# Kernel tuning notes

Hardware: AMD Instinct MI355X
Metric: run time of the kernel (lower is better)

## Reference

```python
import jax, jax.numpy as jnp
import numpy as np

B, S, HID = 2, 1024, 4096
NQ, NG, D = 32, 4, 128
NKV = NQ // NG  # 8 kv heads
OFF = 1024


def setup_inputs() -> dict:
    key = jax.random.key(0)
    ks = jax.random.split(key, 13)
    w = 0.02
    return {
        "x": jax.random.normal(ks[0], (B, S, HID), jnp.float32),
        "offset": OFF,
        "precomp_freqs_cos": jax.random.uniform(ks[1], (S, D // 2), jnp.float32, -1.0, 1.0),
        "precomp_freqs_sin": jax.random.uniform(ks[2], (S, D // 2), jnp.float32, -1.0, 1.0),
        "k_cache": jax.random.normal(ks[3], (B, OFF, NQ, D), jnp.float32),
        "v_cache": jax.random.normal(ks[4], (B, OFF, NQ, D), jnp.float32),
        "q_w": jax.random.normal(ks[5], (NQ * D, HID), jnp.float32) * w,
        "q_b": jax.random.normal(ks[6], (NQ * D,), jnp.float32) * w,
        "k_w": jax.random.normal(ks[7], (NKV * D, HID), jnp.float32) * w,
        "k_b": jax.random.normal(ks[8], (NKV * D,), jnp.float32) * w,
        "v_w": jax.random.normal(ks[9], (NKV * D, HID), jnp.float32) * w,
        "v_b": jax.random.normal(ks[10], (NKV * D,), jnp.float32) * w,
        "o_w": jax.random.normal(ks[11], (HID, NQ * D), jnp.float32) * w,
    }


def _rope(x, cos, sin):
    # x: [b, s, h, d]; cos/sin: [s, d//2] applied to interleaved pairs
    b, s, h, d = x.shape
    xp = x.reshape(b, s, h, d // 2, 2)
    xr, xi = xp[..., 0], xp[..., 1]
    c = cos[None, :, None, :]
    sn = sin[None, :, None, :]
    out = jnp.stack([xr * c - xi * sn, xr * sn + xi * c], axis=-1)
    return out.reshape(b, s, h, d)


def reference(x, offset, precomp_freqs_cos, precomp_freqs_sin, k_cache, v_cache,
              q_w, q_b, k_w, k_b, v_w, v_b, o_w):
    b, s, _ = x.shape
    q = (x @ q_w.T + q_b).reshape(b, s, NQ, D)
    k = (x @ k_w.T + k_b).reshape(b, s, NKV, D)
    v = (x @ v_w.T + v_b).reshape(b, s, NKV, D)
    # GQA expansion: '(hr)' -> each kv head repeated NG times contiguously
    k = jnp.repeat(k, NG, axis=2)  # [b, s, NQ, D]
    v = jnp.repeat(v, NG, axis=2)
    q = _rope(q, precomp_freqs_cos, precomp_freqs_sin)
    k = _rope(k, precomp_freqs_cos, precomp_freqs_sin)
    k = jnp.concatenate([k_cache, k], axis=1)  # [b, offset+s, NQ, D]
    v = jnp.concatenate([v_cache, v], axis=1)
    qk = jnp.einsum('bsnd,btnd->bnst', q, k) / np.float32(np.sqrt(D))
    neg_inf = jnp.asarray(-jnp.inf, qk.dtype)
    causal = jnp.triu(jnp.full((s, s), neg_inf, qk.dtype), k=1)
    mask = jnp.concatenate([jnp.zeros((s, offset), qk.dtype), causal], axis=1)
    qk = qk + mask[None, None, :, :]
    p = jax.nn.softmax(qk, axis=-1)
    out = jnp.einsum('bnst,btnd->bsnd', p, v).reshape(b, s, NQ * D)
    out = out @ o_w.T
    return (out, k, v)
```

## Files before the change

kernel.cpp:

```cpp
#include <hip/hip_runtime.h>
#include <hip/hip_bf16.h>
#include <cstdio>
#include <cstdint>

typedef __bf16 bf16_t;
typedef __bf16 bf16x8 __attribute__((ext_vector_type(8)));
typedef float f32x4 __attribute__((ext_vector_type(4)));

static constexpr int Bc = 2, Sc = 1024, HIDc = 4096;
static constexpr int NQc = 32, NKVc = 8, Dc = 128, OFFc = 1024, Tc = 2048;
static constexpr int Mrows = Bc * Sc;
static constexpr int NQKV = (NQc + 2 * NKVc) * Dc;

__device__ inline void load_lds16(const void* g, void* l) {
    __builtin_amdgcn_global_load_lds(
        (const __attribute__((address_space(1))) unsigned*)g,
        (__attribute__((address_space(3))) unsigned*)l, 16, 0, 0);
}

__global__ void k_cvt(const float* __restrict__ src, bf16_t* __restrict__ dst, long n4) {
    long i = blockIdx.x * (long)blockDim.x + threadIdx.x;
    long stride = (long)gridDim.x * blockDim.x;
    const float4* s4 = (const float4*)src;
    for (; i < n4; i += stride) {
        float4 v = s4[i];
        bf16_t t[4] = {(bf16_t)v.x, (bf16_t)v.y, (bf16_t)v.z, (bf16_t)v.w};
        *(uint2*)&dst[i * 4] = *(uint2*)t;
    }
}

template <bool BIAS, bool OUT_BF16>
__global__ __launch_bounds__(256) void k_gemm(const bf16_t* __restrict__ A,
                                              const bf16_t* __restrict__ Bm,
                                              const float* __restrict__ bias,
                                              void* __restrict__ Cout,
                                              int M, int N, int K) {
    __shared__ __align__(16) bf16_t As[128][32];
    __shared__ __align__(16) bf16_t Bs[128][32];
    const int tid = threadIdx.x, wid = tid >> 6, lane = tid & 63;
    const int g = lane >> 4, ln = lane & 15;
    const int wm = wid >> 1, wn = wid & 1;
    const int gx = gridDim.x;
    int bidl = blockIdx.y * gx + blockIdx.x;
    int cpx = (gx * gridDim.y) >> 3;
    int swz = (bidl & 7) * cpx + (bidl >> 3);
    const int m0 = (swz / gx) * 128, n0 = (swz % gx) * 128;
    f32x4 acc[4][4] = {};

    for (int k0 = 0; k0 < K; k0 += 32) {
        __syncthreads();
#pragma unroll
        for (int c = 0; c < 2; ++c) {
            int row = wid * 32 + c * 16 + (lane >> 2);
            int col = (lane & 3) * 8;
            load_lds16(A + (size_t)(m0 + row) * K + k0 + col, &As[wid * 32 + c * 16][0]);
            load_lds16(Bm + (size_t)(n0 + row) * K + k0 + col, &Bs[wid * 32 + c * 16][0]);
        }
        __syncthreads();
        bf16x8 af[4], bfr[4];
#pragma unroll
        for (int i = 0; i < 4; ++i) af[i] = *(const bf16x8*)&As[wm * 64 + i * 16 + ln][g * 8];
#pragma unroll
        for (int i = 0; i < 4; ++i) bfr[i] = *(const bf16x8*)&Bs[wn * 64 + i * 16 + ln][g * 8];
#pragma unroll
        for (int i = 0; i < 4; ++i)
#pragma unroll
            for (int j = 0; j < 4; ++j)
                acc[i][j] = __builtin_amdgcn_mfma_f32_16x16x32_bf16(af[i], bfr[j], acc[i][j], 0, 0, 0);
    }

#pragma unroll
    for (int i = 0; i < 4; ++i) {
#pragma unroll
        for (int j = 0; j < 4; ++j) {
            int col = n0 + wn * 64 + j * 16 + ln;
            float bv = BIAS ? bias[col] : 0.f;
#pragma unroll
            for (int r = 0; r < 4; ++r) {
                int row = m0 + wm * 64 + i * 16 + g * 4 + r;
                float v = acc[i][j][r] + bv;
                if (OUT_BF16)
                    ((bf16_t*)Cout)[(size_t)row * N + col] = (bf16_t)v;
                else
                    ((float*)Cout)[(size_t)row * N + col] = v;
            }
        }
    }
}

__global__ void k_rope_q(bf16_t* __restrict__ qkv, const float* __restrict__ cosT,
                         const float* __restrict__ sinT) {
    int row = blockIdx.x;
    int s = row & 1023;
    bf16_t* src = qkv + (size_t)row * NQKV;
    for (int p = threadIdx.x; p < 2048; p += 256) {
        int j = p & 63;
        float c = cosT[s * 64 + j], sn = sinT[s * 64 + j];
        float xr = (float)src[2 * p], xi = (float)src[2 * p + 1];
        src[2 * p]     = (bf16_t)(xr * c - xi * sn);
        src[2 * p + 1] = (bf16_t)(xr * sn + xi * c);
    }
}


__global__ __launch_bounds__(256) void k_ropekv(const bf16_t* __restrict__ qkv,
                                                const float* __restrict__ cosT,
                                                const float* __restrict__ sinT,
                                                float* __restrict__ out_k,
                                                float* __restrict__ out_v,
                                                bf16_t* __restrict__ kfr,
                                                bf16_t* __restrict__ vfr) {
    __shared__ __align__(16) bf16_t Vl[64][136];
    const int sb = blockIdx.x, hk = blockIdx.y, b = blockIdx.z;
    const int tid = threadIdx.x;
    const int tt = tid >> 2, dq = (tid & 3) * 32;
    const int s = sb * 64 + tt;
    const int t = OFFc + s;
    const bf16_t* krow = qkv + (size_t)(b * Sc + s) * NQKV + NQc * Dc + hk * Dc + dq;
    const bf16_t* vrow = qkv + (size_t)(b * Sc + s) * NQKV + (NQc + NKVc) * Dc + hk * Dc + dq;

    float cs[16], sn[16];
    int j0 = dq >> 1;
#pragma unroll
    for (int q4 = 0; q4 < 4; ++q4) {
        float4 cv = *(const float4*)&cosT[s * 64 + j0 + q4 * 4];
        float4 sv = *(const float4*)&sinT[s * 64 + j0 + q4 * 4];
        cs[q4 * 4] = cv.x; cs[q4 * 4 + 1] = cv.y; cs[q4 * 4 + 2] = cv.z; cs[q4 * 4 + 3] = cv.w;
        sn[q4 * 4] = sv.x; sn[q4 * 4 + 1] = sv.y; sn[q4 * 4 + 2] = sv.z; sn[q4 * 4 + 3] = sv.w;
    }

    bf16_t kb[32], vb[32];
#pragma unroll
    for (int c = 0; c < 4; ++c) {
        *(uint4*)&kb[c * 8] = *(const uint4*)&krow[c * 8];
        *(uint4*)&vb[c * 8] = *(const uint4*)&vrow[c * 8];
    }
    float ko[32], vo[32];
    bf16_t kbf[32];
#pragma unroll
    for (int jj = 0; jj < 16; ++jj) {
        float xr = (float)kb[2 * jj], xi = (float)kb[2 * jj + 1];
        ko[2 * jj]     = xr * cs[jj] - xi * sn[jj];
        ko[2 * jj + 1] = xr * sn[jj] + xi * cs[jj];
        kbf[2 * jj]     = (bf16_t)ko[2 * jj];
        kbf[2 * jj + 1] = (bf16_t)ko[2 * jj + 1];
        vo[2 * jj] = (float)vb[2 * jj];
        vo[2 * jj + 1] = (float)vb[2 * jj + 1];
    }

    const int t16 = t >> 4, lnr = t & 15, dc = dq >> 5;
#pragma unroll
    for (int gg = 0; gg < 4; ++gg) {
        int hq = hk * 4 + gg;
        size_t o = ((size_t)(b * Tc + t) * NQc + hq) * Dc + dq;
#pragma unroll
        for (int c = 0; c < 8; ++c) {
            *(float4*)&out_k[o + c * 4] = *(float4*)&ko[c * 4];
            *(float4*)&out_v[o + c * 4] = *(float4*)&vo[c * 4];
        }
        size_t fb = ((size_t)b * NQc + hq) * ((size_t)Tc * Dc);
#pragma unroll
        for (int g = 0; g < 4; ++g)
            *(uint4*)&kfr[fb + (size_t)(((t16 * 4 + dc) * 4 + g) * 128 + lnr * 8)] = *(uint4*)&kbf[g * 8];
    }
#pragma unroll
    for (int c = 0; c < 4; ++c) *(uint4*)&Vl[tt][dq + c * 8] = *(uint4*)&vb[c * 8];
    __syncthreads();
    const int tile = 16 + sb;
#pragma unroll
    for (int i = 0; i < 4; ++i) {
        int u = i * 256 + tid;
        int d = u >> 3, cc = u & 7;
        bf16_t tmp[8];
#pragma unroll
        for (int j = 0; j < 8; ++j) tmp[j] = Vl[cc * 8 + j][d];
        size_t off = (size_t)((((tile * 8 + (d >> 4)) * 2 + (cc >> 2)) * 4 + (cc & 3)) * 128 + (d & 15) * 8);
#pragma unroll
        for (int gg = 0; gg < 4; ++gg) {
            int hq = hk * 4 + gg;
            size_t fb = ((size_t)b * NQc + hq) * ((size_t)Tc * Dc);
            *(uint4*)&vfr[fb + off] = *(uint4*)tmp;
        }
    }
}

__global__ __launch_bounds__(256) void k_cache(const float* __restrict__ kc,
                                               const float* __restrict__ vc,
                                               float* __restrict__ out_k,
                                               float* __restrict__ out_v,
                                               bf16_t* __restrict__ kfr,
                                               bf16_t* __restrict__ vfr) {
    __shared__ __align__(16) bf16_t Vl[64][136];
    const int tb = blockIdx.x, h = blockIdx.y, b = blockIdx.z;
    const int tid = threadIdx.x;
    const int tt = tid >> 2, dq = (tid & 3) * 32;
    const int t = tb * 64 + tt;
    size_t src = ((size_t)(b * OFFc + t) * NQc + h) * Dc + dq;
    size_t dst = ((size_t)(b * Tc + t) * NQc + h) * Dc + dq;
    const size_t fb = ((size_t)b * NQc + h) * ((size_t)Tc * Dc);

    bf16_t kb[32], vb[32];
#pragma unroll
    for (int c = 0; c < 8; ++c) {
        float4 kv = *(const float4*)&kc[src + c * 4];
        *(float4*)&out_k[dst + c * 4] = kv;
        kb[c * 4] = (bf16_t)kv.x; kb[c * 4 + 1] = (bf16_t)kv.y;
        kb[c * 4 + 2] = (bf16_t)kv.z; kb[c * 4 + 3] = (bf16_t)kv.w;
        float4 vv = *(const float4*)&vc[src + c * 4];
        *(float4*)&out_v[dst + c * 4] = vv;
        vb[c * 4] = (bf16_t)vv.x; vb[c * 4 + 1] = (bf16_t)vv.y;
        vb[c * 4 + 2] = (bf16_t)vv.z; vb[c * 4 + 3] = (bf16_t)vv.w;
    }
    const int t16 = t >> 4, lnr = t & 15, dc = dq >> 5;
#pragma unroll
    for (int g = 0; g < 4; ++g)
        *(uint4*)&kfr[fb + (size_t)(((t16 * 4 + dc) * 4 + g) * 128 + lnr * 8)] = *(uint4*)&kb[g * 8];

#pragma unroll
    for (int c = 0; c < 4; ++c) *(uint4*)&Vl[tt][dq + c * 8] = *(uint4*)&vb[c * 8];
    __syncthreads();
#pragma unroll
    for (int i = 0; i < 4; ++i) {
        int u = i * 256 + tid;
        int d = u >> 3, cc = u & 7;
        bf16_t tmp[8];
#pragma unroll
        for (int j = 0; j < 8; ++j) tmp[j] = Vl[cc * 8 + j][d];
        size_t off = (size_t)((((tb * 8 + (d >> 4)) * 2 + (cc >> 2)) * 4 + (cc & 3)) * 128 + (d & 15) * 8);
        *(uint4*)&vfr[fb + off] = *(uint4*)tmp;
    }
}

__global__ __launch_bounds__(512) void k_attn(const bf16_t* __restrict__ qkv,
                                              const bf16_t* __restrict__ kfr,
                                              const bf16_t* __restrict__ vfr,
                                              bf16_t* __restrict__ attn) {
    __shared__ __align__(16) bf16_t Kl[2][8192];
    __shared__ __align__(16) bf16_t Vl2[2][8192];
    __shared__ __align__(16) bf16_t Pl[8][32 * 72];
    const int tid = threadIdx.x, w = tid >> 6, l = tid & 63;
    const int g = l >> 4, ln = l & 15;
    const int bid = blockIdx.x;
    const int xcd = bid & 7, within = bid >> 3;
    const int qblk = 3 - (within & 3);
    const int u = within >> 2;
    const int b = u >> 2;
    const int h = (u & 3) * 8 + xcd;
    const int q0b = qblk * 256;
    const int qw0 = q0b + w * 32;
    const float SCALE = 0.08838834764831845f;
    const float L2E = 1.4426950408889634f;
    const size_t hb = ((size_t)b * NQc + h) * ((size_t)Tc * Dc);
    const bf16_t* kb = kfr + hb;
    const bf16_t* vb = vfr + hb;
    bf16_t* Pw = &Pl[w][0];

    bf16x8 qf[2][4];
#pragma unroll
    for (int mf = 0; mf < 2; ++mf) {
        size_t qrow = (size_t)(b * Sc + qw0 + mf * 16 + ln) * NQKV + h * Dc;
#pragma unroll
        for (int dc = 0; dc < 4; ++dc) qf[mf][dc] = *(const bf16x8*)&qkv[qrow + dc * 32 + g * 8];
    }
    f32x4 o[2][8] = {};
    float mrun[2] = {-1e30f, -1e30f};
    float lrun[2] = {0.f, 0.f};

    const int ntiles = (OFFc + q0b + 256) >> 6;

    auto stage = [&](int bf, int t) {
        const bf16_t* ksrc = kb + (size_t)t * 8192 + (size_t)(w * 2) * 512;
        const bf16_t* vsrc = vb + (size_t)t * 8192 + (size_t)(w * 2) * 512;
        load_lds16(ksrc + (size_t)l * 8,       &Kl[bf][(w * 2) * 512]);
        load_lds16(ksrc + 512 + (size_t)l * 8, &Kl[bf][(w * 2 + 1) * 512]);
        load_lds16(vsrc + (size_t)l * 8,       &Vl2[bf][(w * 2) * 512]);
        load_lds16(vsrc + 512 + (size_t)l * 8, &Vl2[bf][(w * 2 + 1) * 512]);
    };

    stage(0, 0);
    __syncthreads();
    int cur = 0;

    for (int t = 0; t < ntiles; ++t) {
        if (t + 1 < ntiles) stage(cur ^ 1, t + 1);
        f32x4 sa[2][4] = {};
#pragma unroll
        for (int nf = 0; nf < 4; ++nf) {
            bf16x8 kf[4];
#pragma unroll
            for (int dc = 0; dc < 4; ++dc)
                kf[dc] = *(const bf16x8*)&Kl[cur][((nf * 4 + dc) * 4 + g) * 128 + ln * 8];
#pragma unroll
            for (int dc = 0; dc < 4; ++dc) {
                sa[0][nf] = __builtin_amdgcn_mfma_f32_16x16x32_bf16(kf[dc], qf[0][dc], sa[0][nf], 0, 0, 0);
                sa[1][nf] = __builtin_amdgcn_mfma_f32_16x16x32_bf16(kf[dc], qf[1][dc], sa[1][nf], 0, 0, 0);
            }
        }
        bool maybe = (t * 64 + 63 > OFFc + qw0);
#pragma unroll
        for (int mf = 0; mf < 2; ++mf)
#pragma unroll
            for (int nf = 0; nf < 4; ++nf)
#pragma unroll
                for (int r = 0; r < 4; ++r) {
                    float s = sa[mf][nf][r] * SCALE;
                    if (maybe) {
                        int tg = t * 64 + nf * 16 + g * 4 + r;
                        int qg = qw0 + mf * 16 + ln;
                        if (tg > OFFc + qg) s = -1e30f;
                    }
                    sa[mf][nf][r] = s;
                }
        float tm[2];
        int grew = 0;
#pragma unroll
        for (int mf = 0; mf < 2; ++mf) {
            float m2 = sa[mf][0][0];
#pragma unroll
            for (int nf = 0; nf < 4; ++nf)
#pragma unroll
                for (int r = 0; r < 4; ++r) m2 = fmaxf(m2, sa[mf][nf][r]);
            m2 = fmaxf(m2, __shfl_xor(m2, 16));
            m2 = fmaxf(m2, __shfl_xor(m2, 32));
            tm[mf] = m2;
            grew |= (m2 > mrun[mf]) ? 1 : 0;
        }
        if (__any(grew)) {
#pragma unroll
            for (int mf = 0; mf < 2; ++mf) {
                float mn = fmaxf(mrun[mf], tm[mf]);
                float al = exp2f((mrun[mf] - mn) * L2E);
                mrun[mf] = mn;
                lrun[mf] *= al;
                float alr[4];
#pragma unroll
                for (int r = 0; r < 4; ++r)
                    alr[r] = __shfl(al, (l & 48) | (g * 4 + r));
#pragma unroll
                for (int df = 0; df < 8; ++df) {
                    f32x4 t4 = o[mf][df];
                    t4[0] *= alr[0]; t4[1] *= alr[1]; t4[2] *= alr[2]; t4[3] *= alr[3];
                    o[mf][df] = t4;
                }
            }
        }
#pragma unroll
        for (int mf = 0; mf < 2; ++mf) {
            const int qrow = mf * 16 + ln;
            float ps = 0.f;
#pragma unroll
            for (int nf = 0; nf < 4; ++nf) {
                bf16_t pv[4];
#pragma unroll
                for (int r = 0; r < 4; ++r) {
                    float p = exp2f((sa[mf][nf][r] - mrun[mf]) * L2E);
                    ps += p;
                    pv[r] = (bf16_t)p;
                }
                *(uint2*)&Pw[qrow * 72 + nf * 16 + g * 4] = *(uint2*)pv;
            }
            ps += __shfl_xor(ps, 16);
            ps += __shfl_xor(ps, 32);
            lrun[mf] += ps;
        }
#pragma unroll
        for (int kc = 0; kc < 2; ++kc) {
            bf16x8 vf[8];
#pragma unroll
            for (int df = 0; df < 8; ++df)
                vf[df] = *(const bf16x8*)&Vl2[cur][((df * 2 + kc) * 4 + g) * 128 + ln * 8];
#pragma unroll
            for (int mf = 0; mf < 2; ++mf) {
                bf16x8 pa = *(const bf16x8*)&Pw[(mf * 16 + ln) * 72 + kc * 32 + g * 8];
#pragma unroll
                for (int df = 0; df < 8; ++df)
                    o[mf][df] = __builtin_amdgcn_mfma_f32_16x16x32_bf16(pa, vf[df], o[mf][df], 0, 0, 0);
            }
        }
        __syncthreads();
        cur ^= 1;
    }

#pragma unroll
    for (int mf = 0; mf < 2; ++mf) {
        float linv[4];
#pragma unroll
        for (int r = 0; r < 4; ++r)
            linv[r] = 1.f / __shfl(lrun[mf], (l & 48) | (g * 4 + r));
#pragma unroll
        for (int df = 0; df < 8; ++df)
#pragma unroll
            for (int r = 0; r < 4; ++r) {
                float v = o[mf][df][r] * linv[r];
                size_t orow = (size_t)(b * Sc + qw0 + mf * 16 + g * 4 + r) * (NQc * Dc) + h * Dc + df * 16 + ln;
                attn[orow] = (bf16_t)v;
            }
    }
}

extern "C" void kernel_launch(void* const* d_in, const int* in_sizes, int n_in,
                              void* d_out, int out_size, void* d_ws, size_t ws_size,
                              hipStream_t stream) {
    const float* x      = (const float*)d_in[0];
    const float* cosT   = (const float*)d_in[2];
    const float* sinT   = (const float*)d_in[3];
    const float* kcache = (const float*)d_in[4];
    const float* vcache = (const float*)d_in[5];
    const float* q_w    = (const float*)d_in[6];
    const float* q_b    = (const float*)d_in[7];
    const float* k_w    = (const float*)d_in[8];
    const float* k_b    = (const float*)d_in[9];
    const float* v_w    = (const float*)d_in[10];
    const float* v_b    = (const float*)d_in[11];
    const float* o_w    = (const float*)d_in[12];

    char* ws = (char*)d_ws;
    size_t off = 0;
    auto alloc = [&](size_t bytes) {
        void* p = ws + off;
        off += (bytes + 255) & ~(size_t)255;
        return p;
    };
    bf16_t* xb   = (bf16_t*)alloc((size_t)Mrows * HIDc * 2);
    bf16_t* wqkv = (bf16_t*)alloc((size_t)Bc * Tc * NQc * Dc * 4);
    bf16_t* owb  = (bf16_t*)alloc((size_t)HIDc * HIDc * 2);
    bf16_t* qkv  = (bf16_t*)alloc((size_t)Mrows * NQKV * 2);
    float*  bias = (float*)alloc((size_t)NQKV * 4);
    if (off > ws_size) {
        fprintf(stderr, "WS too small: need %zu have %zu\n", off, ws_size);
        return;
    }
    bf16_t* attn  = xb;
    bf16_t* kfr = wqkv;
    bf16_t* vfr = wqkv + (size_t)Bc * NQc * Tc * Dc;

    float* out_o = (float*)d_out;
    float* out_k = out_o + (size_t)Mrows * HIDc;
    float* out_v = out_k + (size_t)Bc * Tc * NQc * Dc;

    k_cvt<<<2048, 256, 0, stream>>>(x, xb, (long)Mrows * HIDc / 4);
    k_cvt<<<2048, 256, 0, stream>>>(q_w, wqkv, (long)NQc * Dc * HIDc / 4);
    k_cvt<<<1024, 256, 0, stream>>>(k_w, wqkv + (size_t)NQc * Dc * HIDc, (long)NKVc * Dc * HIDc / 4);
    k_cvt<<<1024, 256, 0, stream>>>(v_w, wqkv + (size_t)(NQc + NKVc) * Dc * HIDc, (long)NKVc * Dc * HIDc / 4);
    k_cvt<<<2048, 256, 0, stream>>>(o_w, owb, (long)HIDc * HIDc / 4);
    (void)hipMemcpyAsync(bias, q_b, (size_t)NQc * Dc * 4, hipMemcpyDeviceToDevice, stream);
    (void)hipMemcpyAsync(bias + NQc * Dc, k_b, (size_t)NKVc * Dc * 4, hipMemcpyDeviceToDevice, stream);
    (void)hipMemcpyAsync(bias + (NQc + NKVc) * Dc, v_b, (size_t)NKVc * Dc * 4, hipMemcpyDeviceToDevice, stream);

    k_gemm<true, true><<<dim3(NQKV / 128, Mrows / 128), 256, 0, stream>>>(
        xb, wqkv, bias, qkv, Mrows, NQKV, HIDc);
    k_rope_q<<<Mrows, 256, 0, stream>>>(qkv, cosT, sinT);
    k_ropekv<<<dim3(16, 8, 2), 256, 0, stream>>>(qkv, cosT, sinT, out_k, out_v, kfr, vfr);
    k_cache<<<dim3(16, 32, 2), 256, 0, stream>>>(kcache, vcache, out_k, out_v, kfr, vfr);
    k_attn<<<256, 512, 0, stream>>>(qkv, kfr, vfr, attn);
    k_gemm<false, false><<<dim3(HIDc / 128, Mrows / 128), 256, 0, stream>>>(
        attn, owb, nullptr, d_out, Mrows, HIDc, HIDc);
}
```

Baseline: 515.6 us.

## Replace GEMM with 8-wave double-buffered 256-row tiles and swizzled LDS

The 128x128 single-buffered GEMM is replaced by a 512-thread kernel with 256xBN tiles and a K-step of 64. Loads for the next tile go directly to LDS into a second buffer while the current tile is computed. LDS addresses are XOR-swizzled to avoid bank conflicts, and MFMA phases run at raised priority. The intent is more data reuse per tile and hiding global load latency, at the cost of more LDS and registers per block, which limits occupancy to one block.

New measurement: 627.4 us. 21.7% more time.

```diff
diff --git a/kernel.cpp b/kernel.cpp
--- a/kernel.cpp
+++ b/kernel.cpp
@@ -29,55 +29,113 @@
     }
 }
 
-template <bool BIAS, bool OUT_BF16>
-__global__ __launch_bounds__(256) void k_gemm(const bf16_t* __restrict__ A,
-                                              const bf16_t* __restrict__ Bm,
-                                              const float* __restrict__ bias,
-                                              void* __restrict__ Cout,
-                                              int M, int N, int K) {
-    __shared__ __align__(16) bf16_t As[128][32];
-    __shared__ __align__(16) bf16_t Bs[128][32];
-    const int tid = threadIdx.x, wid = tid >> 6, lane = tid & 63;
-    const int g = lane >> 4, ln = lane & 15;
-    const int wm = wid >> 1, wn = wid & 1;
+template <int BN, bool BIAS, bool OUT_BF16>
+__global__ __launch_bounds__(512, 1) void k_gemm8(const bf16_t* __restrict__ A,
+                                                  const bf16_t* __restrict__ Bm,
+                                                  const float* __restrict__ bias,
+                                                  void* __restrict__ Cout,
+                                                  int M, int N, int K) {
+    constexpr int NF = BN / 64;
+    constexpr int NBC = BN / 64;
+    __shared__ __align__(16) bf16_t At[2][256 * 64];
+    __shared__ __align__(16) bf16_t Bt[2][BN * 64];
+    const int tid = threadIdx.x, w = tid >> 6, l = tid & 63;
+    const int g = l >> 4, ln = l & 15;
+    const int wm = w >> 2, wn = w & 3;
     const int gx = gridDim.x;
     int bidl = blockIdx.y * gx + blockIdx.x;
     int cpx = (gx * gridDim.y) >> 3;
     int swz = (bidl & 7) * cpx + (bidl >> 3);
-    const int m0 = (swz / gx) * 128, n0 = (swz % gx) * 128;
-    f32x4 acc[4][4] = {};
-
-    for (int k0 = 0; k0 < K; k0 += 32) {
-        __syncthreads();
-#pragma unroll
-        for (int c = 0; c < 2; ++c) {
-            int row = wid * 32 + c * 16 + (lane >> 2);
-            int col = (lane & 3) * 8;
-            load_lds16(A + (size_t)(m0 + row) * K + k0 + col, &As[wid * 32 + c * 16][0]);
-            load_lds16(Bm + (size_t)(n0 + row) * K + k0 + col, &Bs[wid * 32 + c * 16][0]);
-        }
-        __syncthreads();
-        bf16x8 af[4], bfr[4];
-#pragma unroll
-        for (int i = 0; i < 4; ++i) af[i] = *(const bf16x8*)&As[wm * 64 + i * 16 + ln][g * 8];
-#pragma unroll
-        for (int i = 0; i < 4; ++i) bfr[i] = *(const bf16x8*)&Bs[wn * 64 + i * 16 + ln][g * 8];
-#pragma unroll
-        for (int i = 0; i < 4; ++i)
-#pragma unroll
-            for (int j = 0; j < 4; ++j)
-                acc[i][j] = __builtin_amdgcn_mfma_f32_16x16x32_bf16(af[i], bfr[j], acc[i][j], 0, 0, 0);
-    }
-
-#pragma unroll
-    for (int i = 0; i < 4; ++i) {
-#pragma unroll
-        for (int j = 0; j < 4; ++j) {
-            int col = n0 + wn * 64 + j * 16 + ln;
+    const int m0 = (swz / gx) * 256, n0 = (swz % gx) * BN;
+
+    f32x4 acc[8][NF] = {};
+    const int NT = K >> 6;
+
+    auto stageA = [&](int bf, int kt, int c) {
+        int rl = c * 64 + (w << 3) + (l >> 3);
+        const bf16_t* src = A + (size_t)(m0 + rl) * K + kt * 64 + (((l & 7) ^ (rl & 7)) << 3);
+        load_lds16(src, &At[bf][(c * 64 + (w << 3)) * 64]);
+    };
+    auto stageB = [&](int bf, int kt, int c) {
+        int rl = c * 64 + (w << 3) + (l >> 3);
+        const bf16_t* src = Bm + (size_t)(n0 + rl) * K + kt * 64 + (((l & 7) ^ (rl & 7)) << 3);
+        load_lds16(src, &Bt[bf][(c * 64 + (w << 3)) * 64]);
+    };
+
+#pragma unroll
+    for (int c = 0; c < 4; ++c) stageA(0, 0, c);
+#pragma unroll
+    for (int c = 0; c < NBC; ++c) stageB(0, 0, c);
+    asm volatile("s_waitcnt vmcnt(0)" ::: "memory");
+    __builtin_amdgcn_s_barrier();
+
+    int cur = 0;
+    for (int kt = 0; kt < NT; ++kt) {
+        const bool pf = (kt + 1 < NT);
+        bf16x8 bfr[NF][2];
+#pragma unroll
+        for (int p = 0; p < 4; ++p) {
+            if (pf) {
+                if (BN == 256) {
+                    if (p == 0) { stageA(cur ^ 1, kt + 1, 0); stageA(cur ^ 1, kt + 1, 1); stageB(cur ^ 1, kt + 1, 0); }
+                    else if (p == 1) { stageA(cur ^ 1, kt + 1, 2); stageA(cur ^ 1, kt + 1, 3); stageB(cur ^ 1, kt + 1, 1); }
+                    else if (p == 2) { stageB(cur ^ 1, kt + 1, 2); stageB(cur ^ 1, kt + 1, 3); }
+                } else {
+                    if (p == 0) { stageA(cur ^ 1, kt + 1, 0); stageA(cur ^ 1, kt + 1, 1); }
+                    else if (p == 1) { stageA(cur ^ 1, kt + 1, 2); stageA(cur ^ 1, kt + 1, 3); }
+                    else if (p == 2) { stageB(cur ^ 1, kt + 1, 0); if (NBC > 1) stageB(cur ^ 1, kt + 1, 1); }
+                }
+            }
+            if (p == 0) {
+#pragma unroll
+                for (int j = 0; j < NF; ++j) {
+                    int row = wn * (NF * 16) + j * 16 + ln;
+#pragma unroll
+                    for (int kk = 0; kk < 2; ++kk) {
+                        int su = (kk * 4 + g) ^ (row & 7);
+                        bfr[j][kk] = *(const bf16x8*)&Bt[cur][row * 64 + su * 8];
+                    }
+                }
+            }
+            bf16x8 af[2][2];
+#pragma unroll
+            for (int mm = 0; mm < 2; ++mm) {
+                int row = wm * 128 + (p * 2 + mm) * 16 + ln;
+#pragma unroll
+                for (int kk = 0; kk < 2; ++kk) {
+                    int su = (kk * 4 + g) ^ (row & 7);
+                    af[mm][kk] = *(const bf16x8*)&At[cur][row * 64 + su * 8];
+                }
+            }
+            __builtin_amdgcn_s_barrier();
+            asm volatile("s_waitcnt lgkmcnt(0)" ::: "memory");
+            __builtin_amdgcn_sched_barrier(0);
+            __builtin_amdgcn_s_setprio(1);
+#pragma unroll
+            for (int mm = 0; mm < 2; ++mm)
+#pragma unroll
+                for (int j = 0; j < NF; ++j)
+#pragma unroll
+                    for (int kk = 0; kk < 2; ++kk)
+                        acc[p * 2 + mm][j] = __builtin_amdgcn_mfma_f32_16x16x32_bf16(
+                            af[mm][kk], bfr[j][kk], acc[p * 2 + mm][j], 0, 0, 0);
+            __builtin_amdgcn_s_setprio(0);
+            if (p < 3) __builtin_amdgcn_s_barrier();
+        }
+        if (pf) asm volatile("s_waitcnt vmcnt(0)" ::: "memory");
+        __builtin_amdgcn_s_barrier();
+        cur ^= 1;
+    }
+
+#pragma unroll
+    for (int i = 0; i < 8; ++i) {
+#pragma unroll
+        for (int j = 0; j < NF; ++j) {
+            int col = n0 + wn * (NF * 16) + j * 16 + ln;
             float bv = BIAS ? bias[col] : 0.f;
 #pragma unroll
             for (int r = 0; r < 4; ++r) {
-                int row = m0 + wm * 64 + i * 16 + g * 4 + r;
+                int row = m0 + wm * 128 + i * 16 + g * 4 + r;
                 float v = acc[i][j][r] + bv;
                 if (OUT_BF16)
                     ((bf16_t*)Cout)[(size_t)row * N + col] = (bf16_t)v;
@@ -447,12 +505,12 @@
     (void)hipMemcpyAsync(bias + NQc * Dc, k_b, (size_t)NKVc * Dc * 4, hipMemcpyDeviceToDevice, stream);
     (void)hipMemcpyAsync(bias + (NQc + NKVc) * Dc, v_b, (size_t)NKVc * Dc * 4, hipMemcpyDeviceToDevice, stream);
 
-    k_gemm<true, true><<<dim3(NQKV / 128, Mrows / 128), 256, 0, stream>>>(
+    k_gemm8<256, true, true><<<dim3(NQKV / 256, Mrows / 256), 512, 0, stream>>>(
         xb, wqkv, bias, qkv, Mrows, NQKV, HIDc);
     k_rope_q<<<Mrows, 256, 0, stream>>>(qkv, cosT, sinT);
     k_ropekv<<<dim3(16, 8, 2), 256, 0, stream>>>(qkv, cosT, sinT, out_k, out_v, kfr, vfr);
     k_cache<<<dim3(16, 32, 2), 256, 0, stream>>>(kcache, vcache, out_k, out_v, kfr, vfr);
     k_attn<<<256, 512, 0, stream>>>(qkv, kfr, vfr, attn);
-    k_gemm<false, false><<<dim3(HIDc / 128, Mrows / 128), 256, 0, stream>>>(
+    k_gemm8<128, false, false><<<dim3(HIDc / 128, Mrows / 256), 512, 0, stream>>>(
         attn, owb, nullptr, d_out, Mrows, HIDc, HIDc);
 }
```

## Replace GEMM with 256x128 tile, triple-buffered, XOR-swizzled pipelined kernel

Applied to the files above, without the earlier changes.

The bf16 GEMM used for the QKV and output projections is replaced by a 512-thread kernel. It uses 256x128 tiles and a 64-wide K step, and prefetches tiles with direct-to-LDS loads into three LDS buffers, two stages ahead, synchronised with explicit vmcnt waits. LDS columns are XOR-swizzled to avoid bank conflicts, and MFMA blocks run at raised wave priority with interleaved fragment loads. The goal is to hide global memory latency and raise MFMA utilisation. In exchange it uses far more LDS, runs one block per CU, and relies on hand-counted waitcnt values that must match the number of outstanding loads. The epilogue indexing, unchanged and not shown, must still match the new 8-wave layout.

Result: slower. 582.5 us (+13.0%).

```diff
diff --git a/kernel.cpp b/kernel.cpp
--- a/kernel.cpp
+++ b/kernel.cpp
@@ -30,43 +30,102 @@
 }
 
 template <bool BIAS, bool OUT_BF16>
-__global__ __launch_bounds__(256) void k_gemm(const bf16_t* __restrict__ A,
-                                              const bf16_t* __restrict__ Bm,
-                                              const float* __restrict__ bias,
-                                              void* __restrict__ Cout,
-                                              int M, int N, int K) {
-    __shared__ __align__(16) bf16_t As[128][32];
-    __shared__ __align__(16) bf16_t Bs[128][32];
-    const int tid = threadIdx.x, wid = tid >> 6, lane = tid & 63;
-    const int g = lane >> 4, ln = lane & 15;
-    const int wm = wid >> 1, wn = wid & 1;
+__global__ __launch_bounds__(512, 1) void k_gemm3(const bf16_t* __restrict__ A,
+                                                  const bf16_t* __restrict__ Bm,
+                                                  const float* __restrict__ bias,
+                                                  void* __restrict__ Cout,
+                                                  int M, int N, int K) {
+    __shared__ __align__(16) bf16_t At[3][256 * 64];
+    __shared__ __align__(16) bf16_t Bt[3][128 * 64];
+    const int tid = threadIdx.x, w = tid >> 6, l = tid & 63;
+    const int g = l >> 4, ln = l & 15;
+    const int wm = w >> 1, wn = w & 1;
     const int gx = gridDim.x;
     int bidl = blockIdx.y * gx + blockIdx.x;
     int cpx = (gx * gridDim.y) >> 3;
     int swz = (bidl & 7) * cpx + (bidl >> 3);
-    const int m0 = (swz / gx) * 128, n0 = (swz % gx) * 128;
+    const int m0 = (swz / gx) * 256, n0 = (swz % gx) * 128;
+
     f32x4 acc[4][4] = {};
-
-    for (int k0 = 0; k0 < K; k0 += 32) {
-        __syncthreads();
+    const int NT = K >> 6;
+
+    auto stage = [&](int bf, int kt) {
+#pragma unroll
+        for (int c = 0; c < 4; ++c) {
+            int rl = c * 64 + (w << 3) + (l >> 3);
+            load_lds16(A + (size_t)(m0 + rl) * K + kt * 64 + (((l & 7) ^ (rl & 7)) << 3),
+                       &At[bf][(c * 64 + (w << 3)) * 64]);
+        }
 #pragma unroll
         for (int c = 0; c < 2; ++c) {
-            int row = wid * 32 + c * 16 + (lane >> 2);
-            int col = (lane & 3) * 8;
-            load_lds16(A + (size_t)(m0 + row) * K + k0 + col, &As[wid * 32 + c * 16][0]);
-            load_lds16(Bm + (size_t)(n0 + row) * K + k0 + col, &Bs[wid * 32 + c * 16][0]);
-        }
-        __syncthreads();
-        bf16x8 af[4], bfr[4];
-#pragma unroll
-        for (int i = 0; i < 4; ++i) af[i] = *(const bf16x8*)&As[wm * 64 + i * 16 + ln][g * 8];
-#pragma unroll
-        for (int i = 0; i < 4; ++i) bfr[i] = *(const bf16x8*)&Bs[wn * 64 + i * 16 + ln][g * 8];
-#pragma unroll
-        for (int i = 0; i < 4; ++i)
+            int rl = c * 64 + (w << 3) + (l >> 3);
+            load_lds16(Bm + (size_t)(n0 + rl) * K + kt * 64 + (((l & 7) ^ (rl & 7)) << 3),
+                       &Bt[bf][(c * 64 + (w << 3)) * 64]);
+        }
+    };
+
+    stage(0, 0);
+    if (NT > 1) stage(1, 1);
+    if (NT > 1) asm volatile("s_waitcnt vmcnt(6)" ::: "memory");
+    else        asm volatile("s_waitcnt vmcnt(0)" ::: "memory");
+    __builtin_amdgcn_s_barrier();
+
+    for (int kt = 0; kt < NT; ++kt) {
+        const int cur = kt % 3;
+        bf16_t* Ac = &At[cur][0];
+        bf16_t* Bcur = &Bt[cur][0];
+        if (kt + 2 < NT) stage((kt + 2) % 3, kt + 2);
+
+        bf16x8 bfr[4][2], af[2][2];
+#pragma unroll
+        for (int j = 0; j < 4; ++j) {
+            int row = wn * 64 + j * 16 + ln;
+#pragma unroll
+            for (int kk = 0; kk < 2; ++kk)
+                bfr[j][kk] = *(const bf16x8*)&Bcur[row * 64 + (((kk * 4 + g) ^ (row & 7)) << 3)];
+        }
+#pragma unroll
+        for (int mm = 0; mm < 2; ++mm) {
+            int row = wm * 64 + mm * 16 + ln;
+#pragma unroll
+            for (int kk = 0; kk < 2; ++kk)
+                af[mm][kk] = *(const bf16x8*)&Ac[row * 64 + (((kk * 4 + g) ^ (row & 7)) << 3)];
+        }
+        __builtin_amdgcn_s_barrier();
+        __builtin_amdgcn_s_setprio(1);
+#pragma unroll
+        for (int mm = 0; mm < 2; ++mm)
 #pragma unroll
             for (int j = 0; j < 4; ++j)
-                acc[i][j] = __builtin_amdgcn_mfma_f32_16x16x32_bf16(af[i], bfr[j], acc[i][j], 0, 0, 0);
+#pragma unroll
+                for (int kk = 0; kk < 2; ++kk)
+                    acc[mm][j] = __builtin_amdgcn_mfma_f32_16x16x32_bf16(
+                        af[mm][kk], bfr[j][kk], acc[mm][j], 0, 0, 0);
+        __builtin_amdgcn_s_setprio(0);
+
+        bf16x8 af2[2][2];
+#pragma unroll
+        for (int mm = 0; mm < 2; ++mm) {
+            int row = wm * 64 + (2 + mm) * 16 + ln;
+#pragma unroll
+            for (int kk = 0; kk < 2; ++kk)
+                af2[mm][kk] = *(const bf16x8*)&Ac[row * 64 + (((kk * 4 + g) ^ (row & 7)) << 3)];
+        }
+        __builtin_amdgcn_s_barrier();
+        __builtin_amdgcn_s_setprio(1);
+#pragma unroll
+        for (int mm = 0; mm < 2; ++mm)
+#pragma unroll
+            for (int j = 0; j < 4; ++j)
+#pragma unroll
+                for (int kk = 0; kk < 2; ++kk)
+                    acc[2 + mm][j] = __builtin_amdgcn_mfma_f32_16x16x32_bf16(
+                        af2[mm][kk], bfr[j][kk], acc[2 + mm][j], 0, 0, 0);
+        __builtin_amdgcn_s_setprio(0);
+
+        if (kt + 2 < NT)      asm volatile("s_waitcnt vmcnt(6)" ::: "memory");
+        else if (kt + 1 < NT) asm volatile("s_waitcnt vmcnt(0)" ::: "memory");
+        __builtin_amdgcn_s_barrier();
     }
 
 #pragma unroll
@@ -447,12 +506,12 @@
     (void)hipMemcpyAsync(bias + NQc * Dc, k_b, (size_t)NKVc * Dc * 4, hipMemcpyDeviceToDevice, stream);
     (void)hipMemcpyAsync(bias + (NQc + NKVc) * Dc, v_b, (size_t)NKVc * Dc * 4, hipMemcpyDeviceToDevice, stream);
 
-    k_gemm<true, true><<<dim3(NQKV / 128, Mrows / 128), 256, 0, stream>>>(
+    k_gemm3<true, true><<<dim3(NQKV / 128, Mrows / 256), 512, 0, stream>>>(
         xb, wqkv, bias, qkv, Mrows, NQKV, HIDc);
     k_rope_q<<<Mrows, 256, 0, stream>>>(qkv, cosT, sinT);
     k_ropekv<<<dim3(16, 8, 2), 256, 0, stream>>>(qkv, cosT, sinT, out_k, out_v, kfr, vfr);
     k_cache<<<dim3(16, 32, 2), 256, 0, stream>>>(kcache, vcache, out_k, out_v, kfr, vfr);
     k_attn<<<256, 512, 0, stream>>>(qkv, kfr, vfr, attn);
-    k_gemm<false, false><<<dim3(HIDc / 128, Mrows / 128), 256, 0, stream>>>(
+    k_gemm3<false, false><<<dim3(HIDc / 128, Mrows / 256), 512, 0, stream>>>(
         attn, owb, nullptr, d_out, Mrows, HIDc, HIDc);
 }
```
